# Optimization experiments

Measured on AMD Instinct MI355X. Metric: run time of the kernel, lower is better.

The kernel has to match this reference:

```python
import jax, jax.numpy as jnp
import numpy as np

B, S, D, H, E, K = 2, 1024, 1024, 512, 16, 4  # batch, seq, hidden, expert inter, n_experts, top_k
HS = 2 * H  # shared expert inter dim = num_shared_experts * moe_inter_dim


def silu(z):
    return z * jax.nn.sigmoid(z)


def setup_inputs() -> dict:
    key = jax.random.key(0)
    ks = jax.random.split(key, 8)
    sc = lambda fan_in: 1.0 / np.sqrt(fan_in)
    x = jax.random.normal(ks[0], (B, S, D), jnp.float32)
    gate_w = jax.random.normal(ks[1], (E, D), jnp.float32) * sc(D)
    ws_in = jax.random.normal(ks[2], (D, HS), jnp.float32) * sc(D)
    vs_in = jax.random.normal(ks[3], (D, HS), jnp.float32) * sc(D)
    ws_out = jax.random.normal(ks[4], (HS, D), jnp.float32) * sc(HS)
    e_win = jax.random.normal(ks[5], (E, D, H), jnp.float32) * sc(D)
    e_vin = jax.random.normal(ks[6], (E, D, H), jnp.float32) * sc(D)
    e_wout = jax.random.normal(ks[7], (E, H, D), jnp.float32) * sc(H)
    return {"x": x, "gate_w": gate_w, "ws_in": ws_in, "vs_in": vs_in,
            "ws_out": ws_out, "e_win": e_win, "e_vin": e_vin, "e_wout": e_wout}


def reference(x, gate_w, ws_in, vs_in, ws_out, e_win, e_vin, e_wout):
    b, s, d = x.shape
    T = b * s
    xf = x.reshape(T, d)

    # --- Gate (eval path: biases buffer is zero / unused) ---
    g = jax.nn.sigmoid(xf @ gate_w.T)                      # [T, E]
    topv, topi = jax.lax.top_k(g, K)                        # [T, K]
    wn = topv / jnp.sum(topv, axis=-1, keepdims=True)       # normalized top-k weights
    # sparse combine matrix [T, E]: zero for unrouted experts -> exact same math
    # as the original per-expert masked gather/scatter loop
    combine = jnp.zeros_like(g).at[jnp.arange(T)[:, None], topi].add(wn)

    # --- Routed experts (SwiGLU), batched over experts ---
    hin = jnp.einsum('td,edh->eth', xf, e_win)              # [E, T, H]
    vin = jnp.einsum('td,edh->eth', xf, e_vin)              # [E, T, H]
    h = silu(hin) * vin * combine.T[:, :, None]             # weight before down-proj
    routed = jnp.einsum('eth,ehd->td', h, e_wout)           # [T, D]

    # --- Shared expert (SwiGLU with inter = num_shared * moe_inter) ---
    shared = (silu(xf @ ws_in) * (xf @ vs_in)) @ ws_out     # [T, D]

    return (shared + routed).reshape(b, s, d)
```

## Files before the change

### kernel.cpp

```cpp
#include <hip/hip_runtime.h>
#include <hip/hip_bf16.h>
#include <math.h>

typedef __attribute__((ext_vector_type(4))) float f32x4;
typedef __attribute__((ext_vector_type(8))) short s16x8;
typedef __hip_bfloat16 bf16;

constexpr int TOK = 2048;
constexpr int DIM = 1024;
constexpr int HID = 512;
constexpr int NE  = 16;
constexpr int NK  = 4;
constexpr int NHS = 1024;
constexpr int NPAIR = TOK * NK;

constexpr int UP_GRID = 256 + 4 * 144;
constexpr int DN_GRID = 128 + 4 * 144;

#define MFMA(a, b, c) __builtin_amdgcn_mfma_f32_16x16x32_bf16(a, b, c, 0, 0, 0)

#define GLOAD_LDS(gp, lp)                                                        \
  __builtin_amdgcn_global_load_lds(                                              \
      (const __attribute__((address_space(1))) unsigned int*)(gp),               \
      (__attribute__((address_space(3))) unsigned int*)(lp), 16, 0, 0)

template <int CH>
static __device__ __forceinline__ void stage_p(const bf16* const* rp, int k0,
                                               bf16* lds, int tid) {
  int wid = tid >> 6;
#pragma unroll
  for (int i = 0; i < CH; ++i) {
    int c = i * 512 + tid;
    int row = c >> 3;
    int slot = c & 7;
    int j = slot ^ (row & 7);
    const bf16* g = rp[i] + k0 + j * 8;
    bf16* l = lds + (size_t)(i * 512 + wid * 64) * 8;
    GLOAD_LDS(g, l);
  }
}

static __device__ __forceinline__ s16x8 frag(const bf16* lds, int row, int kc) {
  return *(const s16x8*)(lds + row * 64 + ((kc ^ (row & 7)) << 3));
}

static __device__ __forceinline__ float b2f(short u) {
  union { unsigned int i; float f; } c;
  c.i = ((unsigned int)(unsigned short)u) << 16;
  return c.f;
}

struct bf16x4 { bf16 a, b, c, d; };


static __device__ __forceinline__ void tr_tile(const float* __restrict__ src,
                                               bf16* __restrict__ dst, int R, int C,
                                               int bx, int by, float t[32][33], int tid) {
  int tx = tid & 31, ty = tid >> 5;
  int c0 = bx * 32, r0 = by * 32;
#pragma unroll
  for (int i = 0; i < 32; i += 8) t[ty + i][tx] = src[(size_t)(r0 + ty + i) * C + c0 + tx];
  __syncthreads();
#pragma unroll
  for (int i = 0; i < 32; i += 8)
    dst[(size_t)(c0 + ty + i) * R + r0 + tx] = __float2bfloat16(t[tx][ty + i]);
}

__global__ __launch_bounds__(256) void prep1(const float* __restrict__ ws_in,
                                             const float* __restrict__ vs_in,
                                             const float* __restrict__ e_win,
                                             const float* __restrict__ e_vin,
                                             bf16* __restrict__ wsinT, bf16* __restrict__ vsinT,
                                             bf16* __restrict__ ewinT, bf16* __restrict__ evinT) {
  __shared__ float t[32][33];
  int bid = blockIdx.x, tid = threadIdx.x;
  if (bid < 1024) {
    tr_tile(ws_in, wsinT, DIM, NHS, bid & 31, bid >> 5, t, tid);
  } else if (bid < 2048) {
    int b = bid - 1024;
    tr_tile(vs_in, vsinT, DIM, NHS, b & 31, b >> 5, t, tid);
  } else if (bid < 10240) {
    int b = bid - 2048, e = b >> 9; b &= 511;
    tr_tile(e_win + (size_t)e * DIM * HID, ewinT + (size_t)e * DIM * HID,
            DIM, HID, b & 15, b >> 4, t, tid);
  } else {
    int b = bid - 10240, e = b >> 9; b &= 511;
    tr_tile(e_vin + (size_t)e * DIM * HID, evinT + (size_t)e * DIM * HID,
            DIM, HID, b & 15, b >> 4, t, tid);
  }
}

__global__ __launch_bounds__(256) void prep2(const float* __restrict__ ws_out,
                                             const float* __restrict__ e_wout,
                                             bf16* __restrict__ wsoutT,
                                             bf16* __restrict__ ewoutT) {
  __shared__ float t[32][33];
  int bid = blockIdx.x, tid = threadIdx.x;
  if (bid < 1024) {
    tr_tile(ws_out, wsoutT, NHS, DIM, bid & 31, bid >> 5, t, tid);
  } else {
    int b = bid - 1024, e = b >> 9; b &= 511;
    tr_tile(e_wout + (size_t)e * HID * DIM, ewoutT + (size_t)e * HID * DIM,
            HID, DIM, b & 31, b >> 5, t, tid);
  }
}


__global__ __launch_bounds__(256) void gate_scores(const float* __restrict__ x,
                                                   const float* __restrict__ gw,
                                                   bf16* __restrict__ xb,
                                                   float* __restrict__ scores) {
  int lane = threadIdx.x & 63, wid = threadIdx.x >> 6;
  int t = blockIdx.x * 4 + wid;
  const float* xr = x + (size_t)t * DIM + lane * 16;
  float4 x4[4];
#pragma unroll
  for (int q = 0; q < 4; ++q) x4[q] = *(const float4*)(xr + q * 4);
  {
    bf16* xo = xb + (size_t)t * DIM + lane * 16;
#pragma unroll
    for (int q = 0; q < 4; ++q) {
      bf16x4 o{__float2bfloat16(x4[q].x), __float2bfloat16(x4[q].y),
               __float2bfloat16(x4[q].z), __float2bfloat16(x4[q].w)};
      *reinterpret_cast<bf16x4*>(xo + q * 4) = o;
    }
  }
  float s[NE];
#pragma unroll
  for (int e = 0; e < NE; ++e) {
    const float* wr_ = gw + (size_t)e * DIM + lane * 16;
    float a = 0.f;
#pragma unroll
    for (int q = 0; q < 4; ++q) {
      float4 w4 = *(const float4*)(wr_ + q * 4);
      a += x4[q].x * w4.x + x4[q].y * w4.y + x4[q].z * w4.z + x4[q].w * w4.w;
    }
    s[e] = a;
  }
#pragma unroll
  for (int e = 0; e < NE; ++e)
#pragma unroll
    for (int off = 32; off; off >>= 1) s[e] += __shfl_xor(s[e], off);
  if (lane == 0) {
#pragma unroll
    for (int e = 0; e < NE; ++e) scores[(size_t)t * NE + e] = s[e];
  }
}

__global__ __launch_bounds__(256) void topk_hist(const float* __restrict__ scores,
                                                 int* __restrict__ topi,
                                                 float* __restrict__ topw,
                                                 int* __restrict__ counts) {
  __shared__ int h[NE];
  int tid = threadIdx.x;
  int t = blockIdx.x * 256 + tid;
  if (tid < NE) h[tid] = 0;
  __syncthreads();
  float g[NE];
  const float* sr = scores + (size_t)t * NE;
#pragma unroll
  for (int q = 0; q < 4; ++q) {
    float4 v = *(const float4*)(sr + q * 4);
    g[q * 4 + 0] = 1.f / (1.f + expf(-v.x));
    g[q * 4 + 1] = 1.f / (1.f + expf(-v.y));
    g[q * 4 + 2] = 1.f / (1.f + expf(-v.z));
    g[q * 4 + 3] = 1.f / (1.f + expf(-v.w));
  }
  unsigned used = 0;
  int bi[NK]; float bv[NK];
  float sum = 0.f;
#pragma unroll
  for (int j = 0; j < NK; ++j) {
    int best = 0; float v = -1e30f;
#pragma unroll
    for (int e = 0; e < NE; ++e)
      if (!((used >> e) & 1u) && g[e] > v) { v = g[e]; best = e; }
    used |= 1u << best; bi[j] = best; bv[j] = v; sum += v;
  }
  float inv = 1.f / sum;
#pragma unroll
  for (int j = 0; j < NK; ++j) {
    topi[t * NK + j] = bi[j];
    topw[t * NK + j] = bv[j] * inv;
    atomicAdd(&h[bi[j]], 1);
  }
  __syncthreads();
  if (tid < NE) atomicAdd(&counts[tid], h[tid]);
}

__global__ __launch_bounds__(64) void route_small(const int* __restrict__ counts,
                                                  int* __restrict__ offs,
                                                  int* __restrict__ segs,
                                                  int* __restrict__ nseg,
                                                  int* __restrict__ cursor) {
  if (threadIdx.x != 0) return;
  int o = 0;
#pragma unroll
  for (int e = 0; e < NE; ++e) { offs[e] = o; cursor[e * 32] = 0; o += counts[e]; }
  int s = 0;
  for (int e = 0; e < NE; ++e)
    for (int m = 0; m < counts[e]; m += 64) segs[s++] = (e << 16) | m;
  nseg[0] = s;
}

__global__ __launch_bounds__(256) void scatter_pairs(const int* __restrict__ topi,
                                                     const float* __restrict__ topw,
                                                     const int* __restrict__ offs,
                                                     int* __restrict__ cursor,
                                                     int* __restrict__ tok_list,
                                                     float* __restrict__ w_list,
                                                     int* __restrict__ pair_slot) {
  int p = blockIdx.x * 256 + threadIdx.x;
  if (p >= NPAIR) return;
  int e = topi[p];
  int rank = atomicAdd(&cursor[e * 32], 1);
  int slot = offs[e] + rank;
  tok_list[slot] = p >> 2;
  w_list[slot] = topw[p];
  pair_slot[p] = slot;
}


__global__ __launch_bounds__(512, 4) void up_all(
    const bf16* __restrict__ xb, const bf16* __restrict__ wsinT,
    const bf16* __restrict__ vsinT, const bf16* __restrict__ ewinT,
    const bf16* __restrict__ evinT, const int* __restrict__ tok_list,
    const float* __restrict__ w_list, const int* __restrict__ counts,
    const int* __restrict__ offs, const int* __restrict__ segs,
    const int* __restrict__ nseg, bf16* __restrict__ hsb,
    bf16* __restrict__ hre) {
  int bid = blockIdx.x;
  int j = (bid & 7) * (UP_GRID / 8) + (bid >> 3);
  int nj = 256 + 4 * nseg[0];
  if (j >= nj) return;
  int tid = threadIdx.x, lane = tid & 63, w = tid >> 6;

  bool is_shared = (j < 256);
  int m0, n0, cnt = TOK, off_e = 0;
  const bf16 *w1, *w2;
  if (is_shared) {
    m0 = (j >> 3) * 64; n0 = j & 7;
    w1 = wsinT; w2 = vsinT;
  } else {
    int r = j - 256;
    int sv = segs[r >> 2]; n0 = r & 3;
    int e = sv >> 16; m0 = sv & 0xffff;
    cnt = counts[e]; off_e = offs[e];
    w1 = ewinT + (size_t)e * HID * DIM;
    w2 = evinT + (size_t)e * HID * DIM;
  }

  const bf16* ap[1]; const bf16* bp[4];
  {
    int row = tid >> 3;
    int gr = is_shared ? (m0 + row) : tok_list[off_e + min(m0 + row, cnt - 1)];
    ap[0] = xb + (size_t)gr * DIM;
  }
#pragma unroll
  for (int i = 0; i < 4; ++i) {
    int r = (i * 512 + tid) >> 3;
    int ridx = n0 * 128 + (r >> 5) * 16 + (r & 15);
    bp[i] = ((r & 16) ? w2 : w1) + (size_t)ridx * DIM;
  }

  __shared__ alignas(16) bf16 As[2][64 * 64], Bs[2][256 * 64];
  f32x4 acc[4][2];
  f32x4 z4 = {0.f, 0.f, 0.f, 0.f};
#pragma unroll
  for (int m = 0; m < 4; ++m) { acc[m][0] = z4; acc[m][1] = z4; }

  constexpr int NT = DIM / 64;
  stage_p<1>(ap, 0, As[0], tid);
  stage_p<4>(bp, 0, Bs[0], tid);
  stage_p<1>(ap, 64, As[1], tid);
  stage_p<4>(bp, 64, Bs[1], tid);

  for (int kt = 0; kt < NT; ++kt) {
    int cur = kt & 1;
    if (kt + 1 < NT) asm volatile("s_waitcnt vmcnt(5)" ::: "memory");
    else             asm volatile("s_waitcnt vmcnt(0)" ::: "memory");
    __builtin_amdgcn_sched_barrier(0);
    __builtin_amdgcn_s_barrier();
    __builtin_amdgcn_sched_barrier(0);
    const bf16* Ac = As[cur]; const bf16* Bc = Bs[cur];
#pragma unroll
    for (int ks = 0; ks < 2; ++ks) {
      int r16 = lane & 15, kc = (ks << 2) + (lane >> 4);
      s16x8 a[4];
#pragma unroll
      for (int m = 0; m < 4; ++m) a[m] = frag(Ac, m * 16 + r16, kc);
#pragma unroll
      for (int q = 0; q < 2; ++q) {
        s16x8 b = frag(Bc, w * 32 + q * 16 + r16, kc);
#pragma unroll
        for (int m = 0; m < 4; ++m) acc[m][q] = MFMA(a[m], b, acc[m][q]);
      }
    }
    __builtin_amdgcn_s_barrier();
    __builtin_amdgcn_sched_barrier(0);
    if (kt + 2 < NT) {
      stage_p<1>(ap, (kt + 2) * 64, As[cur], tid);
      stage_p<4>(bp, (kt + 2) * 64, Bs[cur], tid);
    }
  }

  int c = n0 * 128 + w * 16 + (lane & 15);
#pragma unroll
  for (int m = 0; m < 4; ++m)
#pragma unroll
    for (int i = 0; i < 4; ++i) {
      int r = m * 16 + (lane >> 4) * 4 + i;
      float z = acc[m][0][i], v = acc[m][1][i];
      float h = z / (1.f + __expf(-z)) * v;
      if (is_shared) {
        hsb[(size_t)(m0 + r) * NHS + c] = __float2bfloat16(h);
      } else {
        int gr = m0 + r;
        if (gr < cnt)
          hre[(size_t)(off_e + gr) * HID + c] =
              __float2bfloat16(h * w_list[off_e + gr]);
      }
    }
}


__global__ __launch_bounds__(512, 4) void down_all(
    const bf16* __restrict__ hsb, const bf16* __restrict__ wsoutT,
    const bf16* __restrict__ hre, const bf16* __restrict__ ewoutT,
    const int* __restrict__ tok_list, const int* __restrict__ counts,
    const int* __restrict__ offs, const int* __restrict__ segs,
    const int* __restrict__ nseg, float* __restrict__ out,
    bf16* __restrict__ hrd) {
  int bid = blockIdx.x;
  int j = (bid & 7) * (DN_GRID / 8) + (bid >> 3);
  int nj = 128 + 4 * nseg[0];
  if (j >= nj) return;
  int tid = threadIdx.x, lane = tid & 63, w = tid >> 6;

  bool is_shared = (j < 128);
  int m0, n0, cnt = TOK, off_e = 0, K, ldA, ldB;
  const bf16 *Abase, *Bbase;
  if (is_shared) {
    m0 = (j >> 2) * 64; n0 = j & 3;
    Abase = hsb; ldA = NHS; K = NHS;
    Bbase = wsoutT; ldB = NHS;
  } else {
    int r = j - 128;
    int sv = segs[r >> 2]; n0 = r & 3;
    int e = sv >> 16; m0 = sv & 0xffff;
    cnt = counts[e]; off_e = offs[e];
    Abase = hre + (size_t)off_e * HID; ldA = HID; K = HID;
    Bbase = ewoutT + (size_t)e * DIM * HID; ldB = HID;
  }

  const bf16* ap[1]; const bf16* bp[4];
  {
    int row = tid >> 3;
    int gr = is_shared ? (m0 + row) : min(m0 + row, cnt - 1);
    ap[0] = Abase + (size_t)gr * ldA;
  }
#pragma unroll
  for (int i = 0; i < 4; ++i) {
    int r = (i * 512 + tid) >> 3;
    bp[i] = Bbase + (size_t)(n0 * 256 + r) * ldB;
  }

  __shared__ alignas(16) bf16 As[2][64 * 64], Bs[2][256 * 64];
  f32x4 acc[4][2];
  f32x4 z4 = {0.f, 0.f, 0.f, 0.f};
#pragma unroll
  for (int m = 0; m < 4; ++m) { acc[m][0] = z4; acc[m][1] = z4; }

  int NT = K / 64;
  stage_p<1>(ap, 0, As[0], tid);
  stage_p<4>(bp, 0, Bs[0], tid);
  stage_p<1>(ap, 64, As[1], tid);
  stage_p<4>(bp, 64, Bs[1], tid);

  for (int kt = 0; kt < NT; ++kt) {
    int cur = kt & 1;
    if (kt + 1 < NT) asm volatile("s_waitcnt vmcnt(5)" ::: "memory");
    else             asm volatile("s_waitcnt vmcnt(0)" ::: "memory");
    __builtin_amdgcn_sched_barrier(0);
    __builtin_amdgcn_s_barrier();
    __builtin_amdgcn_sched_barrier(0);
    const bf16* Ac = As[cur]; const bf16* Bc = Bs[cur];
#pragma unroll
    for (int ks = 0; ks < 2; ++ks) {
      int r16 = lane & 15, kc = (ks << 2) + (lane >> 4);
      s16x8 a[4];
#pragma unroll
      for (int m = 0; m < 4; ++m) a[m] = frag(Ac, m * 16 + r16, kc);
#pragma unroll
      for (int q = 0; q < 2; ++q) {
        s16x8 b = frag(Bc, w * 32 + q * 16 + r16, kc);
#pragma unroll
        for (int m = 0; m < 4; ++m) acc[m][q] = MFMA(a[m], b, acc[m][q]);
      }
    }
    __builtin_amdgcn_s_barrier();
    __builtin_amdgcn_sched_barrier(0);
    if (kt + 2 < NT) {
      stage_p<1>(ap, (kt + 2) * 64, As[cur], tid);
      stage_p<4>(bp, (kt + 2) * 64, Bs[cur], tid);
    }
  }

#pragma unroll
  for (int q = 0; q < 2; ++q) {
    int c = n0 * 256 + w * 32 + q * 16 + (lane & 15);
#pragma unroll
    for (int m = 0; m < 4; ++m)
#pragma unroll
      for (int i = 0; i < 4; ++i) {
        int r = m * 16 + (lane >> 4) * 4 + i;
        if (is_shared) {
          out[(size_t)(m0 + r) * DIM + c] = acc[m][q][i];
        } else {
          int gr = m0 + r;
          if (gr < cnt)
            hrd[(size_t)(off_e + gr) * DIM + c] = __float2bfloat16(acc[m][q][i]);
        }
      }
  }
}


__global__ __launch_bounds__(256) void finish_add(const bf16* __restrict__ hrd,
                                                  const int* __restrict__ pair_slot,
                                                  float* __restrict__ out) {
  int idx = blockIdx.x * 256 + threadIdx.x;
  int t = idx >> 7;
  int c0 = (idx & 127) * 8;
  int4 s4 = *(const int4*)(pair_slot + t * 4);
  float acc[8];
  float* o = out + (size_t)t * DIM + c0;
#pragma unroll
  for (int k = 0; k < 8; ++k) acc[k] = o[k];
  int sl[4] = {s4.x, s4.y, s4.z, s4.w};
#pragma unroll
  for (int j = 0; j < 4; ++j) {
    s16x8 v = *(const s16x8*)(hrd + (size_t)sl[j] * DIM + c0);
#pragma unroll
    for (int k = 0; k < 8; ++k) acc[k] += b2f(v[k]);
  }
#pragma unroll
  for (int k = 0; k < 8; ++k) o[k] = acc[k];
}


extern "C" void kernel_launch(void* const* d_in, const int* in_sizes, int n_in,
                              void* d_out, int out_size, void* d_ws, size_t ws_size,
                              hipStream_t stream) {
  const float* x      = (const float*)d_in[0];
  const float* gw     = (const float*)d_in[1];
  const float* ws_in  = (const float*)d_in[2];
  const float* vs_in  = (const float*)d_in[3];
  const float* ws_out = (const float*)d_in[4];
  const float* e_win  = (const float*)d_in[5];
  const float* e_vin  = (const float*)d_in[6];
  const float* e_wout = (const float*)d_in[7];
  float* out = (float*)d_out;

  char* p = (char*)d_ws;
  bf16* xb     = (bf16*)p;  p += (size_t)TOK * DIM * 2;
  bf16* wsinT  = (bf16*)p;
  bf16* wsoutT = wsinT;
  p += (size_t)NHS * DIM * 2;
  bf16* vsinT  = (bf16*)p;  p += (size_t)NHS * DIM * 2;
  bf16* hsb    = (bf16*)p;  p += (size_t)TOK * NHS * 2;
  bf16* ewinT  = (bf16*)p;
  bf16* ewoutT = ewinT;
  p += (size_t)NE * DIM * HID * 2;
  bf16* evinT  = (bf16*)p;
  bf16* hrd    = evinT;
  p += (size_t)NE * DIM * HID * 2;
  bf16* hre    = (bf16*)p;  p += (size_t)(NPAIR + 128) * HID * 2;
  int*   topi      = (int*)p;    p += (size_t)NPAIR * 4;
  float* topw      = (float*)p;  p += (size_t)NPAIR * 4;
  int*   tok_list  = (int*)p;    p += (size_t)NPAIR * 4;
  float* w_list    = (float*)p;  p += (size_t)NPAIR * 4;
  int*   pair_slot = (int*)p;    p += (size_t)NPAIR * 4;
  float* scores    = (float*)p;  p += (size_t)TOK * NE * 4;
  int*   counts    = (int*)p;    p += 64;
  int*   offs      = (int*)p;    p += 64;
  int*   cursor    = (int*)p;    p += NE * 32 * 4;
  int*   segs      = (int*)p;    p += 256 * 4;
  int*   nseg      = (int*)p;    p += 64;

  hipMemsetAsync(counts, 0, NE * sizeof(int), stream);
  gate_scores<<<TOK / 4, 256, 0, stream>>>(x, gw, xb, scores);
  topk_hist<<<TOK / 256, 256, 0, stream>>>(scores, topi, topw, counts);
  route_small<<<1, 64, 0, stream>>>(counts, offs, segs, nseg, cursor);
  scatter_pairs<<<NPAIR / 256, 256, 0, stream>>>(topi, topw, offs, cursor,
                                                 tok_list, w_list, pair_slot);

  prep1<<<18432, 256, 0, stream>>>(ws_in, vs_in, e_win, e_vin,
                                   wsinT, vsinT, ewinT, evinT);

  up_all<<<UP_GRID, 512, 0, stream>>>(xb, wsinT, vsinT, ewinT, evinT, tok_list,
                                      w_list, counts, offs, segs, nseg, hsb, hre);

  prep2<<<9216, 256, 0, stream>>>(ws_out, e_wout, wsoutT, ewoutT);

  down_all<<<DN_GRID, 512, 0, stream>>>(hsb, wsoutT, hre, ewoutT, tok_list,
                                        counts, offs, segs, nseg, out, hrd);
  finish_add<<<TOK * DIM / 8 / 256, 256, 0, stream>>>(hrd, pair_slot, out);
}
```

Measured before the change: 153.5 us.

## Retile MoE GEMMs to 128x128 wave grid and widen weight transpose tiles

The up and down GEMMs move from 64-row by 256-column tiles to 128x128 tiles with a 2x4 wave layout. Expert segments grow to 128 rows to match, and s_setprio is raised around the MFMA block. The weight transpose kernels switch from 32x32 to 64x64 tiles with float4 loads and 16-byte bf16 stores, which cuts block count and makes memory accesses wider. Larger expert segments may waste more padded rows for experts whose counts are not multiples of 128, and the bigger LDS footprint may lower occupancy.

```diff
diff --git a/kernel.cpp b/kernel.cpp
--- a/kernel.cpp
+++ b/kernel.cpp
@@ -14,8 +14,8 @@
 constexpr int NHS = 1024;
 constexpr int NPAIR = TOK * NK;
 
-constexpr int UP_GRID = 256 + 4 * 144;
-constexpr int DN_GRID = 128 + 4 * 144;
+constexpr int UP_GRID = 256 + 8 * 80;
+constexpr int DN_GRID = 128 + 8 * 80;
 
 #define MFMA(a, b, c) __builtin_amdgcn_mfma_f32_16x16x32_bf16(a, b, c, 0, 0, 0)
 
@@ -51,19 +51,32 @@
 }
 
 struct bf16x4 { bf16 a, b, c, d; };
-
-
-static __device__ __forceinline__ void tr_tile(const float* __restrict__ src,
-                                               bf16* __restrict__ dst, int R, int C,
-                                               int bx, int by, float t[32][33], int tid) {
-  int tx = tid & 31, ty = tid >> 5;
-  int c0 = bx * 32, r0 = by * 32;
-#pragma unroll
-  for (int i = 0; i < 32; i += 8) t[ty + i][tx] = src[(size_t)(r0 + ty + i) * C + c0 + tx];
+struct alignas(16) bf16x8 { bf16 v[8]; };
+
+
+static __device__ __forceinline__ void tr64(const float* __restrict__ src,
+                                            bf16* __restrict__ dst, int R, int C,
+                                            int bx, int by, float (*t)[65], int tid) {
+  int r0 = by * 64, c0 = bx * 64;
+#pragma unroll
+  for (int i = 0; i < 4; ++i) {
+    int row = i * 16 + (tid >> 4);
+    int col = (tid & 15) * 4;
+    float4 v = *(const float4*)(src + (size_t)(r0 + row) * C + c0 + col);
+    t[row][col] = v.x; t[row][col + 1] = v.y;
+    t[row][col + 2] = v.z; t[row][col + 3] = v.w;
+  }
   __syncthreads();
-#pragma unroll
-  for (int i = 0; i < 32; i += 8)
-    dst[(size_t)(c0 + ty + i) * R + r0 + tx] = __float2bfloat16(t[tx][ty + i]);
+  int c = tid >> 2;
+  int rb = (tid & 3) * 16;
+  bf16x8 o0, o1;
+#pragma unroll
+  for (int k = 0; k < 8; ++k) o0.v[k] = __float2bfloat16(t[rb + k][c]);
+#pragma unroll
+  for (int k = 0; k < 8; ++k) o1.v[k] = __float2bfloat16(t[rb + 8 + k][c]);
+  bf16* d = dst + (size_t)(c0 + c) * R + r0 + rb;
+  *(bf16x8*)d = o0;
+  *(bf16x8*)(d + 8) = o1;
 }
 
 __global__ __launch_bounds__(256) void prep1(const float* __restrict__ ws_in,
@@ -72,21 +85,21 @@
                                              const float* __restrict__ e_vin,
                                              bf16* __restrict__ wsinT, bf16* __restrict__ vsinT,
                                              bf16* __restrict__ ewinT, bf16* __restrict__ evinT) {
-  __shared__ float t[32][33];
+  __shared__ float t[64][65];
   int bid = blockIdx.x, tid = threadIdx.x;
-  if (bid < 1024) {
-    tr_tile(ws_in, wsinT, DIM, NHS, bid & 31, bid >> 5, t, tid);
-  } else if (bid < 2048) {
-    int b = bid - 1024;
-    tr_tile(vs_in, vsinT, DIM, NHS, b & 31, b >> 5, t, tid);
-  } else if (bid < 10240) {
-    int b = bid - 2048, e = b >> 9; b &= 511;
-    tr_tile(e_win + (size_t)e * DIM * HID, ewinT + (size_t)e * DIM * HID,
-            DIM, HID, b & 15, b >> 4, t, tid);
+  if (bid < 256) {
+    tr64(ws_in, wsinT, DIM, NHS, bid & 15, bid >> 4, t, tid);
+  } else if (bid < 512) {
+    int b = bid - 256;
+    tr64(vs_in, vsinT, DIM, NHS, b & 15, b >> 4, t, tid);
+  } else if (bid < 2560) {
+    int b = bid - 512, e = b >> 7; b &= 127;
+    tr64(e_win + (size_t)e * DIM * HID, ewinT + (size_t)e * DIM * HID,
+         DIM, HID, b & 7, b >> 3, t, tid);
   } else {
-    int b = bid - 10240, e = b >> 9; b &= 511;
-    tr_tile(e_vin + (size_t)e * DIM * HID, evinT + (size_t)e * DIM * HID,
-            DIM, HID, b & 15, b >> 4, t, tid);
+    int b = bid - 2560, e = b >> 7; b &= 127;
+    tr64(e_vin + (size_t)e * DIM * HID, evinT + (size_t)e * DIM * HID,
+         DIM, HID, b & 7, b >> 3, t, tid);
   }
 }
 
@@ -94,14 +107,14 @@
                                              const float* __restrict__ e_wout,
                                              bf16* __restrict__ wsoutT,
                                              bf16* __restrict__ ewoutT) {
-  __shared__ float t[32][33];
+  __shared__ float t[64][65];
   int bid = blockIdx.x, tid = threadIdx.x;
-  if (bid < 1024) {
-    tr_tile(ws_out, wsoutT, NHS, DIM, bid & 31, bid >> 5, t, tid);
+  if (bid < 256) {
+    tr64(ws_out, wsoutT, NHS, DIM, bid & 15, bid >> 4, t, tid);
   } else {
-    int b = bid - 1024, e = b >> 9; b &= 511;
-    tr_tile(e_wout + (size_t)e * HID * DIM, ewoutT + (size_t)e * HID * DIM,
-            HID, DIM, b & 31, b >> 5, t, tid);
+    int b = bid - 256, e = b >> 7; b &= 127;
+    tr64(e_wout + (size_t)e * HID * DIM, ewoutT + (size_t)e * HID * DIM,
+         HID, DIM, b & 15, b >> 4, t, tid);
   }
 }
 
@@ -199,7 +212,7 @@
   for (int e = 0; e < NE; ++e) { offs[e] = o; cursor[e * 32] = 0; o += counts[e]; }
   int s = 0;
   for (int e = 0; e < NE; ++e)
-    for (int m = 0; m < counts[e]; m += 64) segs[s++] = (e << 16) | m;
+    for (int m = 0; m < counts[e]; m += 128) segs[s++] = (e << 16) | m;
   nseg[0] = s;
 }
 
@@ -231,85 +244,89 @@
     bf16* __restrict__ hre) {
   int bid = blockIdx.x;
   int j = (bid & 7) * (UP_GRID / 8) + (bid >> 3);
-  int nj = 256 + 4 * nseg[0];
+  int nj = 256 + 8 * nseg[0];
   if (j >= nj) return;
-  int tid = threadIdx.x, lane = tid & 63, w = tid >> 6;
+  int tid = threadIdx.x, lane = tid & 63, wid = tid >> 6;
+  int wr = wid >> 2, wc = wid & 3;
 
   bool is_shared = (j < 256);
   int m0, n0, cnt = TOK, off_e = 0;
   const bf16 *w1, *w2;
   if (is_shared) {
-    m0 = (j >> 3) * 64; n0 = j & 7;
+    m0 = (j >> 4) * 128; n0 = j & 15;
     w1 = wsinT; w2 = vsinT;
   } else {
     int r = j - 256;
-    int sv = segs[r >> 2]; n0 = r & 3;
+    int sv = segs[r >> 3]; n0 = r & 7;
     int e = sv >> 16; m0 = sv & 0xffff;
     cnt = counts[e]; off_e = offs[e];
     w1 = ewinT + (size_t)e * HID * DIM;
     w2 = evinT + (size_t)e * HID * DIM;
   }
 
-  const bf16* ap[1]; const bf16* bp[4];
-  {
-    int row = tid >> 3;
+  const bf16* ap[2]; const bf16* bp[2];
+#pragma unroll
+  for (int i = 0; i < 2; ++i) {
+    int row = (i * 512 + tid) >> 3;
     int gr = is_shared ? (m0 + row) : tok_list[off_e + min(m0 + row, cnt - 1)];
-    ap[0] = xb + (size_t)gr * DIM;
-  }
-#pragma unroll
-  for (int i = 0; i < 4; ++i) {
+    ap[i] = xb + (size_t)gr * DIM;
+  }
+#pragma unroll
+  for (int i = 0; i < 2; ++i) {
     int r = (i * 512 + tid) >> 3;
-    int ridx = n0 * 128 + (r >> 5) * 16 + (r & 15);
+    int ridx = n0 * 64 + (r >> 5) * 16 + (r & 15);
     bp[i] = ((r & 16) ? w2 : w1) + (size_t)ridx * DIM;
   }
 
-  __shared__ alignas(16) bf16 As[2][64 * 64], Bs[2][256 * 64];
+  __shared__ alignas(16) bf16 As[2][128 * 64], Bs[2][128 * 64];
   f32x4 acc[4][2];
   f32x4 z4 = {0.f, 0.f, 0.f, 0.f};
 #pragma unroll
   for (int m = 0; m < 4; ++m) { acc[m][0] = z4; acc[m][1] = z4; }
 
   constexpr int NT = DIM / 64;
-  stage_p<1>(ap, 0, As[0], tid);
-  stage_p<4>(bp, 0, Bs[0], tid);
-  stage_p<1>(ap, 64, As[1], tid);
-  stage_p<4>(bp, 64, Bs[1], tid);
+  stage_p<2>(ap, 0, As[0], tid);
+  stage_p<2>(bp, 0, Bs[0], tid);
+  stage_p<2>(ap, 64, As[1], tid);
+  stage_p<2>(bp, 64, Bs[1], tid);
 
   for (int kt = 0; kt < NT; ++kt) {
     int cur = kt & 1;
-    if (kt + 1 < NT) asm volatile("s_waitcnt vmcnt(5)" ::: "memory");
+    if (kt + 1 < NT) asm volatile("s_waitcnt vmcnt(4)" ::: "memory");
     else             asm volatile("s_waitcnt vmcnt(0)" ::: "memory");
     __builtin_amdgcn_sched_barrier(0);
     __builtin_amdgcn_s_barrier();
     __builtin_amdgcn_sched_barrier(0);
     const bf16* Ac = As[cur]; const bf16* Bc = Bs[cur];
+    __builtin_amdgcn_s_setprio(1);
 #pragma unroll
     for (int ks = 0; ks < 2; ++ks) {
       int r16 = lane & 15, kc = (ks << 2) + (lane >> 4);
       s16x8 a[4];
 #pragma unroll
-      for (int m = 0; m < 4; ++m) a[m] = frag(Ac, m * 16 + r16, kc);
+      for (int m = 0; m < 4; ++m) a[m] = frag(Ac, wr * 64 + m * 16 + r16, kc);
 #pragma unroll
       for (int q = 0; q < 2; ++q) {
-        s16x8 b = frag(Bc, w * 32 + q * 16 + r16, kc);
+        s16x8 b = frag(Bc, wc * 32 + q * 16 + r16, kc);
 #pragma unroll
         for (int m = 0; m < 4; ++m) acc[m][q] = MFMA(a[m], b, acc[m][q]);
       }
     }
+    __builtin_amdgcn_s_setprio(0);
     __builtin_amdgcn_s_barrier();
     __builtin_amdgcn_sched_barrier(0);
     if (kt + 2 < NT) {
-      stage_p<1>(ap, (kt + 2) * 64, As[cur], tid);
-      stage_p<4>(bp, (kt + 2) * 64, Bs[cur], tid);
-    }
-  }
-
-  int c = n0 * 128 + w * 16 + (lane & 15);
+      stage_p<2>(ap, (kt + 2) * 64, As[cur], tid);
+      stage_p<2>(bp, (kt + 2) * 64, Bs[cur], tid);
+    }
+  }
+
+  int c = n0 * 64 + wc * 16 + (lane & 15);
 #pragma unroll
   for (int m = 0; m < 4; ++m)
 #pragma unroll
     for (int i = 0; i < 4; ++i) {
-      int r = m * 16 + (lane >> 4) * 4 + i;
+      int r = wr * 64 + m * 16 + (lane >> 4) * 4 + i;
       float z = acc[m][0][i], v = acc[m][1][i];
       float h = z / (1.f + __expf(-z)) * v;
       if (is_shared) {
@@ -333,87 +350,91 @@
     bf16* __restrict__ hrd) {
   int bid = blockIdx.x;
   int j = (bid & 7) * (DN_GRID / 8) + (bid >> 3);
-  int nj = 128 + 4 * nseg[0];
+  int nj = 128 + 8 * nseg[0];
   if (j >= nj) return;
-  int tid = threadIdx.x, lane = tid & 63, w = tid >> 6;
+  int tid = threadIdx.x, lane = tid & 63, wid = tid >> 6;
+  int wr = wid >> 2, wc = wid & 3;
 
   bool is_shared = (j < 128);
   int m0, n0, cnt = TOK, off_e = 0, K, ldA, ldB;
   const bf16 *Abase, *Bbase;
   if (is_shared) {
-    m0 = (j >> 2) * 64; n0 = j & 3;
+    m0 = (j >> 3) * 128; n0 = j & 7;
     Abase = hsb; ldA = NHS; K = NHS;
     Bbase = wsoutT; ldB = NHS;
   } else {
     int r = j - 128;
-    int sv = segs[r >> 2]; n0 = r & 3;
+    int sv = segs[r >> 3]; n0 = r & 7;
     int e = sv >> 16; m0 = sv & 0xffff;
     cnt = counts[e]; off_e = offs[e];
     Abase = hre + (size_t)off_e * HID; ldA = HID; K = HID;
     Bbase = ewoutT + (size_t)e * DIM * HID; ldB = HID;
   }
 
-  const bf16* ap[1]; const bf16* bp[4];
-  {
-    int row = tid >> 3;
+  const bf16* ap[2]; const bf16* bp[2];
+#pragma unroll
+  for (int i = 0; i < 2; ++i) {
+    int row = (i * 512 + tid) >> 3;
     int gr = is_shared ? (m0 + row) : min(m0 + row, cnt - 1);
-    ap[0] = Abase + (size_t)gr * ldA;
-  }
-#pragma unroll
-  for (int i = 0; i < 4; ++i) {
+    ap[i] = Abase + (size_t)gr * ldA;
+  }
+#pragma unroll
+  for (int i = 0; i < 2; ++i) {
     int r = (i * 512 + tid) >> 3;
-    bp[i] = Bbase + (size_t)(n0 * 256 + r) * ldB;
-  }
-
-  __shared__ alignas(16) bf16 As[2][64 * 64], Bs[2][256 * 64];
+    bp[i] = Bbase + (size_t)(n0 * 128 + r) * ldB;
+  }
+
+  __shared__ alignas(16) bf16 As[2][128 * 64], Bs[2][128 * 64];
   f32x4 acc[4][2];
   f32x4 z4 = {0.f, 0.f, 0.f, 0.f};
 #pragma unroll
   for (int m = 0; m < 4; ++m) { acc[m][0] = z4; acc[m][1] = z4; }
 
   int NT = K / 64;
-  stage_p<1>(ap, 0, As[0], tid);
-  stage_p<4>(bp, 0, Bs[0], tid);
-  stage_p<1>(ap, 64, As[1], tid);
-  stage_p<4>(bp, 64, Bs[1], tid);
+  stage_p<2>(ap, 0, As[0], tid);
+  stage_p<2>(bp, 0, Bs[0], tid);
+  stage_p<2>(ap, 64, As[1], tid);
+  stage_p<2>(bp, 64, Bs[1], tid);
 
   for (int kt = 0; kt < NT; ++kt) {
     int cur = kt & 1;
-    if (kt + 1 < NT) asm volatile("s_waitcnt vmcnt(5)" ::: "memory");
+    if (kt + 1 < NT) asm volatile("s_waitcnt vmcnt(4)" ::: "memory");
     else             asm volatile("s_waitcnt vmcnt(0)" ::: "memory");
     __builtin_amdgcn_sched_barrier(0);
     __builtin_amdgcn_s_barrier();
     __builtin_amdgcn_sched_barrier(0);
     const bf16* Ac = As[cur]; const bf16* Bc = Bs[cur];
+    __builtin_amdgcn_s_setprio(1);
 #pragma unroll
     for (int ks = 0; ks < 2; ++ks) {
       int r16 = lane & 15, kc = (ks << 2) + (lane >> 4);
       s16x8 a[4];
 #pragma unroll
-      for (int m = 0; m < 4; ++m) a[m] = frag(Ac, m * 16 + r16, kc);
+      for (int m = 0; m < 4; ++m) a[m] = frag(Ac, wr * 64 + m * 16 + r16, kc);
 #pragma unroll
       for (int q = 0; q < 2; ++q) {
-        s16x8 b = frag(Bc, w * 32 + q * 16 + r16, kc);
+        s16x8 b = frag(Bc, wc * 32 + q * 16 + r16, kc);
 #pragma unroll
         for (int m = 0; m < 4; ++m) acc[m][q] = MFMA(a[m], b, acc[m][q]);
       }
     }
+    __builtin_amdgcn_s_setprio(0);
     __builtin_amdgcn_s_barrier();
     __builtin_amdgcn_sched_barrier(0);
     if (kt + 2 < NT) {
-      stage_p<1>(ap, (kt + 2) * 64, As[cur], tid);
-      stage_p<4>(bp, (kt + 2) * 64, Bs[cur], tid);
+      stage_p<2>(ap, (kt + 2) * 64, As[cur], tid);
+      stage_p<2>(bp, (kt + 2) * 64, Bs[cur], tid);
     }
   }
 
 #pragma unroll
   for (int q = 0; q < 2; ++q) {
-    int c = n0 * 256 + w * 32 + q * 16 + (lane & 15);
+    int c = n0 * 128 + wc * 32 + q * 16 + (lane & 15);
 #pragma unroll
     for (int m = 0; m < 4; ++m)
 #pragma unroll
       for (int i = 0; i < 4; ++i) {
-        int r = m * 16 + (lane >> 4) * 4 + i;
+        int r = wr * 64 + m * 16 + (lane >> 4) * 4 + i;
         if (is_shared) {
           out[(size_t)(m0 + r) * DIM + c] = acc[m][q][i];
         } else {
@@ -485,7 +506,7 @@
   int*   counts    = (int*)p;    p += 64;
   int*   offs      = (int*)p;    p += 64;
   int*   cursor    = (int*)p;    p += NE * 32 * 4;
-  int*   segs      = (int*)p;    p += 256 * 4;
+  int*   segs      = (int*)p;    p += 128 * 4;
   int*   nseg      = (int*)p;    p += 64;
 
   hipMemsetAsync(counts, 0, NE * sizeof(int), stream);
@@ -495,13 +516,13 @@
   scatter_pairs<<<NPAIR / 256, 256, 0, stream>>>(topi, topw, offs, cursor,
                                                  tok_list, w_list, pair_slot);
 
-  prep1<<<18432, 256, 0, stream>>>(ws_in, vs_in, e_win, e_vin,
-                                   wsinT, vsinT, ewinT, evinT);
+  prep1<<<4608, 256, 0, stream>>>(ws_in, vs_in, e_win, e_vin,
+                                  wsinT, vsinT, ewinT, evinT);
 
   up_all<<<UP_GRID, 512, 0, stream>>>(xb, wsinT, vsinT, ewinT, evinT, tok_list,
                                       w_list, counts, offs, segs, nseg, hsb, hre);
 
-  prep2<<<9216, 256, 0, stream>>>(ws_out, e_wout, wsoutT, ewoutT);
+  prep2<<<2304, 256, 0, stream>>>(ws_out, e_wout, wsoutT, ewoutT);
 
   down_all<<<DN_GRID, 512, 0, stream>>>(hsb, wsoutT, hre, ewoutT, tok_list,
                                         counts, offs, segs, nseg, out, hrd);
```

After: 158.6 us. +3.3%, slower.
